# Optimization experiments

Measured on AMD Instinct MI355X. Metric: run time of the kernel, lower is better.

## Reference

```python
import jax, jax.numpy as jnp
import numpy as np

B, S, E, H = 4, 2048, 1024, 16
D = E // H  # head dim = 64


def setup_inputs() -> dict:
    key = jax.random.key(0)
    ks = jax.random.split(key, 9)
    sc = 1.0 / np.sqrt(E)
    x = jax.random.normal(ks[0], (B, S, E), dtype=jnp.float32)
    # causal mask: 1 = keep, 0 = masked -> -inf (matches masked_fill(mask==0, -inf))
    mask = jnp.broadcast_to(jnp.tril(jnp.ones((S, S), dtype=jnp.int32)), (B, S, S))
    return {
        "x": x,
        "mask": mask,
        "wq": jax.random.normal(ks[1], (E, E), dtype=jnp.float32) * sc,
        "bq": jax.random.normal(ks[2], (E,), dtype=jnp.float32) * sc,
        "wk": jax.random.normal(ks[3], (E, E), dtype=jnp.float32) * sc,
        "bk": jax.random.normal(ks[4], (E,), dtype=jnp.float32) * sc,
        "wv": jax.random.normal(ks[5], (E, E), dtype=jnp.float32) * sc,
        "bv": jax.random.normal(ks[6], (E,), dtype=jnp.float32) * sc,
        "wo": jax.random.normal(ks[7], (E, E), dtype=jnp.float32) * sc,
        "bo": jax.random.normal(ks[8], (E,), dtype=jnp.float32) * sc,
    }


def reference(x, mask, wq, bq, wk, bk, wv, bv, wo, bo):
    # nn.Linear: y = x @ W^T + b
    def proj(w, b):
        y = jnp.einsum('bse,fe->bsf', x, w) + b
        return y.reshape(B, S, H, D).transpose(0, 2, 1, 3)  # [B,H,S,D]

    q = proj(wq, bq)
    k = proj(wk, bk)
    v = proj(wv, bv)
    denom = jnp.asarray(np.sqrt(D), dtype=x.dtype)
    score = jnp.einsum('bhqd,bhkd->bhqk', q, k) / denom  # [B,H,S,S]
    score = jnp.where(mask[:, None, :, :] == 0, jnp.asarray(-jnp.inf, score.dtype), score)
    attn = jax.nn.softmax(score, axis=-1)
    out = jnp.einsum('bhqk,bhkd->bhqd', attn, v)  # [B,H,S,D]
    out = out.transpose(0, 2, 1, 3).reshape(B, S, E)
    return jnp.einsum('bse,fe->bsf', out, wo) + bo
```

## Files before the change

### kernel.cpp

```cpp
#include <hip/hip_runtime.h>
#include <cstdint>
#include <cstddef>

typedef unsigned short u16;
typedef __bf16 bf16;
typedef bf16 bf16x8 __attribute__((ext_vector_type(8)));
typedef bf16 bf16x4 __attribute__((ext_vector_type(4)));
typedef float f32x4 __attribute__((ext_vector_type(4)));
typedef u16 u16x8 __attribute__((ext_vector_type(8)));
typedef u16 u16x4 __attribute__((ext_vector_type(4)));

#define ASYNC16(g, l) __builtin_amdgcn_global_load_lds( \
    (const __attribute__((address_space(1))) void*)(g), \
    (__attribute__((address_space(3))) void*)(l), 16, 0, 0)

__device__ __forceinline__ u16 f2bf(float f) {
  bf16 h = (bf16)f;
  return __builtin_bit_cast(u16, h);
}

__device__ __forceinline__ u16x4 pk4(float a, float b, float c, float d) {
  bf16x4 v = { (bf16)a, (bf16)b, (bf16)c, (bf16)d };
  return __builtin_bit_cast(u16x4, v);
}

__device__ __forceinline__ void store_out(u16* p, float v) { *p = f2bf(v); }
__device__ __forceinline__ void store_out(float* p, float v) { *p = v; }

__device__ __forceinline__ f32x4 mfma16(bf16x8 a, bf16x8 b, f32x4 c) {
  return __builtin_amdgcn_mfma_f32_16x16x32_bf16(a, b, c, 0, 0, 0);
}

__global__ void prep(const float* __restrict__ x,  const float* __restrict__ wq,
                     const float* __restrict__ wk, const float* __restrict__ wv,
                     const float* __restrict__ wo, const float* __restrict__ bq,
                     const float* __restrict__ bk,
                     u16* __restrict__ xb, u16* __restrict__ wqkb,
                     u16* __restrict__ wvb, u16* __restrict__ wob,
                     float* __restrict__ bqk, float scl)
{
  const int bid = blockIdx.x, tid = threadIdx.x;
  if (bid < 8192) {
    int i = bid * 256 + tid;
    float4 v = ((const float4*)x)[i];
    ((u16x4*)xb)[i] = pk4(v.x, v.y, v.z, v.w);
  } else if (bid < 12288) {
    int wsel = (bid - 8192) >> 10;
    int i = ((bid - 8192) & 1023) * 256 + tid;
    const float* src = wsel == 0 ? wq : wsel == 1 ? wk : wsel == 2 ? wv : wo;
    u16* dst = wsel == 0 ? wqkb : wsel == 1 ? wqkb + 1048576 : wsel == 2 ? wvb : wob;
    float s = wsel == 0 ? scl : 1.0f;
    float4 v = ((const float4*)src)[i];
    ((u16x4*)dst)[i] = pk4(v.x * s, v.y * s, v.z * s, v.w * s);
  } else {
    for (int i = tid; i < 1024; i += 256) {
      bqk[i] = bq[i] * scl;
      bqk[1024 + i] = bk[i];
    }
  }
}

template <typename OutT>
__global__ __launch_bounds__(256, 2) void gemm_bt(
    const u16* __restrict__ A, const u16* __restrict__ Bm,
    const float* __restrict__ bias_col, const float* __restrict__ bias_row,
    OutT* __restrict__ C, int M, int N, int K)
{
  __shared__ u16 As[128 * 32];
  __shared__ u16 Bs[128 * 32];
  const int tid = threadIdx.x;
  const int w = tid >> 6, lane = tid & 63;
  const int q = lane >> 4, l15 = lane & 15;
  const int bm = blockIdx.x, bn = blockIdx.y;
  const int wr = w >> 1, wc = w & 1;

  const u16* gA = A + (size_t)(bm * 128 + w * 32 + (lane >> 2)) * K + (lane & 3) * 8;
  const u16* gB = Bm + (size_t)(bn * 128 + w * 32 + (lane >> 2)) * K + (lane & 3) * 8;
  u16* lA = As + w * 32 * 32;
  u16* lB = Bs + w * 32 * 32;

  f32x4 acc[4][4] = {};

  for (int k0 = 0; k0 < K; k0 += 32) {
    ASYNC16(gA + k0,          lA);
    ASYNC16(gA + k0 + 16 * K, lA + 16 * 32);
    ASYNC16(gB + k0,          lB);
    ASYNC16(gB + k0 + 16 * K, lB + 16 * 32);
    __syncthreads();
    bf16x8 af[4], bfr[4];
#pragma unroll
    for (int mt = 0; mt < 4; mt++)
      af[mt] = *(const bf16x8*)(As + (wr * 64 + mt * 16 + l15) * 32 + q * 8);
#pragma unroll
    for (int nt = 0; nt < 4; nt++)
      bfr[nt] = *(const bf16x8*)(Bs + (wc * 64 + nt * 16 + l15) * 32 + q * 8);
#pragma unroll
    for (int mt = 0; mt < 4; mt++)
#pragma unroll
      for (int nt = 0; nt < 4; nt++)
        acc[mt][nt] = mfma16(af[mt], bfr[nt], acc[mt][nt]);
    __syncthreads();
  }

#pragma unroll
  for (int nt = 0; nt < 4; nt++) {
    int c = bn * 128 + wc * 64 + nt * 16 + l15;
    float bc = bias_col ? bias_col[c] : 0.f;
#pragma unroll
    for (int mt = 0; mt < 4; mt++) {
      int r0 = bm * 128 + wr * 64 + mt * 16 + q * 4;
      f32x4 v = acc[mt][nt];
#pragma unroll
      for (int ri = 0; ri < 4; ri++) {
        float bv = bc + (bias_row ? bias_row[r0 + ri] : 0.f);
        store_out(&C[(size_t)(r0 + ri) * N + c], v[ri] + bv);
      }
    }
  }
}

__global__ __launch_bounds__(256, 2) void fattn(
    const u16* __restrict__ QK, const u16* __restrict__ VT, u16* __restrict__ ctx)
{
  __shared__ u16 Kt[128 * 64];
  __shared__ u16 Vt[64 * 128];

  const int tid = threadIdx.x;
  const int w = tid >> 6, lane = tid & 63;
  const int quad = lane >> 4, l15 = lane & 15;
  const int bx = blockIdx.x, h = blockIdx.y, b = blockIdx.z;
  const int base = (b & 2) << 2;
  const int tq = (b & 1) ? ((15 - bx + base) & 15) : ((bx + base) & 15);
  const int qbase = tq * 128 + w * 32;

  const int kr0 = tid >> 3, kcol = (tid & 7) ^ (kr0 & 7);
  const int vr0 = tid >> 4, vcol = (tid & 15) ^ (vr0 & 15);

  const u16* QKb = QK + (size_t)b * 2048 * 2048;
  const u16* Kg = QKb + 1024 + h * 64 + kcol * 8;
  const u16* Vg = VT + (size_t)(h * 64) * 8192 + b * 2048 + vcol * 8;

  u16* Pw = Kt + w * 2048;

  bf16x8 ones;
#pragma unroll
  for (int j = 0; j < 8; j++) ones[j] = (bf16)1.0f;

  bf16x8 qf[2][2];
#pragma unroll
  for (int mt = 0; mt < 2; mt++)
#pragma unroll
    for (int ks = 0; ks < 2; ks++)
      qf[mt][ks] = *(const bf16x8*)(QKb + (size_t)(qbase + mt * 16 + l15) * 2048 +
                                    h * 64 + ks * 32 + quad * 8);

  f32x4 oacc[4][2] = {};
  f32x4 lacc[2] = {};

  for (int t = 0; t <= tq; t++) {
    __syncthreads();
#pragma unroll
    for (int s = 0; s < 4; s++) {
      ASYNC16(Kg + (size_t)(t * 128 + s * 32 + kr0) * 2048, Kt + (s * 256 + w * 64) * 8);
      ASYNC16(Vg + (size_t)(s * 16 + vr0) * 8192 + t * 128, Vt + (s * 256 + w * 64) * 8);
    }
    __syncthreads();

    f32x4 st[2][8] = {};
#pragma unroll
    for (int ks = 0; ks < 2; ks++) {
      bf16x8 kf[8];
#pragma unroll
      for (int nt = 0; nt < 8; nt++) {
        int row = nt * 16 + l15;
        kf[nt] = *(const bf16x8*)(Kt + (row * 8 + ((ks * 4 + quad) ^ (row & 7))) * 8);
      }
#pragma unroll
      for (int nt = 0; nt < 8; nt++) {
        st[0][nt] = mfma16(kf[nt], qf[0][ks], st[0][nt]);
        st[1][nt] = mfma16(kf[nt], qf[1][ks], st[1][nt]);
      }
    }

    if (t == tq) {
#pragma unroll
      for (int mt = 0; mt < 2; mt++) {
        const int qg = qbase + mt * 16 + l15;
#pragma unroll
        for (int nt = 0; nt < 8; nt++)
#pragma unroll
          for (int r = 0; r < 4; r++)
            if (t * 128 + nt * 16 + quad * 4 + r > qg) st[mt][nt][r] = -3e38f;
      }
    }
#pragma unroll
    for (int mt = 0; mt < 2; mt++)
#pragma unroll
      for (int nt = 0; nt < 8; nt++)
#pragma unroll
        for (int r = 0; r < 4; r++)
          st[mt][nt][r] = exp2f(st[mt][nt][r]);

    __syncthreads();

#pragma unroll
    for (int hf = 0; hf < 2; hf++) {
#pragma unroll
      for (int mt = 0; mt < 2; mt++) {
        const int row = mt * 16 + l15;
#pragma unroll
        for (int n2 = 0; n2 < 4; n2++) {
          int nt = hf * 4 + n2;
          u16x4 pk = pk4(st[mt][nt][0], st[mt][nt][1], st[mt][nt][2], st[mt][nt][3]);
          int c = n2 * 2 + (quad >> 1);
          *(u16x4*)(Pw + (row << 6) + ((c ^ (row & 7)) << 3) + ((quad & 1) << 2)) = pk;
        }
      }
#pragma unroll
      for (int ks = 0; ks < 2; ks++) {
        const int c = ks * 4 + quad;
        bf16x8 pf0 = *(const bf16x8*)(Pw + (l15 << 6) + ((c ^ (l15 & 7)) << 3));
        bf16x8 pf1 = *(const bf16x8*)(Pw + ((16 + l15) << 6) + ((c ^ (l15 & 7)) << 3));
        lacc[0] = mfma16(ones, pf0, lacc[0]);
        lacc[1] = mfma16(ones, pf1, lacc[1]);
#pragma unroll
        for (int dt = 0; dt < 4; dt++) {
          int row = dt * 16 + l15;
          bf16x8 vf = *(const bf16x8*)(Vt + (row * 16 + ((hf * 8 + ks * 4 + quad) ^ (row & 15))) * 8);
          oacc[dt][0] = mfma16(vf, pf0, oacc[dt][0]);
          oacc[dt][1] = mfma16(vf, pf1, oacc[dt][1]);
        }
      }
    }
  }

#pragma unroll
  for (int mt = 0; mt < 2; mt++) {
    float rl = 1.0f / lacc[mt][0];
    size_t row = (size_t)b * 2048 + qbase + mt * 16 + l15;
#pragma unroll
    for (int dt = 0; dt < 4; dt++) {
      u16x4 o = pk4(oacc[dt][mt][0] * rl, oacc[dt][mt][1] * rl,
                    oacc[dt][mt][2] * rl, oacc[dt][mt][3] * rl);
      *(u16x4*)(ctx + row * 1024 + h * 64 + dt * 16 + quad * 4) = o;
    }
  }
}

extern "C" void kernel_launch(void* const* d_in, const int* in_sizes, int n_in,
                              void* d_out, int out_size, void* d_ws, size_t ws_size,
                              hipStream_t stream)
{
  const float* x  = (const float*)d_in[0];
  const float* wq = (const float*)d_in[2];
  const float* bq = (const float*)d_in[3];
  const float* wk = (const float*)d_in[4];
  const float* bk = (const float*)d_in[5];
  const float* wv = (const float*)d_in[6];
  const float* bv = (const float*)d_in[7];
  const float* wo = (const float*)d_in[8];
  const float* bo = (const float*)d_in[9];

  const float SCL = 0.125f * 1.44269504088896f;

  char* ws = (char*)d_ws;
  u16*   xb   = (u16*)(ws);
  u16*   ctx  = (u16*)(ws);
  u16*   wqkb = (u16*)(ws + 16777216);
  u16*   wvb  = (u16*)(ws + 20971520);
  u16*   wob  = (u16*)(ws + 23068672);
  float* bqk  = (float*)(ws + 25165824);
  u16*   qk   = (u16*)(ws + 25174016);
  u16*   vt   = (u16*)(ws + 58728448);
  float* out  = (float*)d_out;

  prep<<<12289, 256, 0, stream>>>(x, wq, wk, wv, wo, bq, bk,
                                  xb, wqkb, wvb, wob, bqk, SCL);

  gemm_bt<u16><<<dim3(64, 16), 256, 0, stream>>>(xb, wqkb, bqk, nullptr, qk, 8192, 2048, 1024);
  gemm_bt<u16><<<dim3(8, 64), 256, 0, stream>>>(wvb, xb, nullptr, bv, vt, 1024, 8192, 1024);
  fattn<<<dim3(16, 16, 4), 256, 0, stream>>>(qk, vt, ctx);
  gemm_bt<float><<<dim3(64, 8), 256, 0, stream>>>(ctx, wob, bo, nullptr, out, 8192, 1024, 1024);
}
```

Before: 338.1 us.

## Merge QK and V projection GEMMs into one launch; widen attention blocks to 8 waves

```diff
diff --git a/kernel.cpp b/kernel.cpp
--- a/kernel.cpp
+++ b/kernel.cpp
@@ -61,17 +61,15 @@
 }
 
 template <typename OutT>
-__global__ __launch_bounds__(256, 2) void gemm_bt(
+__device__ __forceinline__ void gemm_core(
+    u16* As, u16* Bs,
     const u16* __restrict__ A, const u16* __restrict__ Bm,
     const float* __restrict__ bias_col, const float* __restrict__ bias_row,
-    OutT* __restrict__ C, int M, int N, int K)
-{
-  __shared__ u16 As[128 * 32];
-  __shared__ u16 Bs[128 * 32];
+    OutT* __restrict__ C, int M, int N, int K, int bm, int bn)
+{
   const int tid = threadIdx.x;
   const int w = tid >> 6, lane = tid & 63;
   const int q = lane >> 4, l15 = lane & 15;
-  const int bm = blockIdx.x, bn = blockIdx.y;
   const int wr = w >> 1, wc = w & 1;
 
   const u16* gA = A + (size_t)(bm * 128 + w * 32 + (lane >> 2)) * K + (lane & 3) * 8;
@@ -119,28 +117,59 @@
   }
 }
 
-__global__ __launch_bounds__(256, 2) void fattn(
+template <typename OutT>
+__global__ __launch_bounds__(256, 2) void gemm_bt(
+    const u16* __restrict__ A, const u16* __restrict__ Bm,
+    const float* __restrict__ bias_col, const float* __restrict__ bias_row,
+    OutT* __restrict__ C, int M, int N, int K)
+{
+  __shared__ u16 As[128 * 32];
+  __shared__ u16 Bs[128 * 32];
+  gemm_core<OutT>(As, Bs, A, Bm, bias_col, bias_row, C, M, N, K,
+                  blockIdx.x, blockIdx.y);
+}
+
+__global__ __launch_bounds__(256, 2) void gemm_qkv(
+    const u16* __restrict__ xb, const u16* __restrict__ wqkb,
+    const u16* __restrict__ wvb, const float* __restrict__ bqk,
+    const float* __restrict__ bv, u16* __restrict__ qk, u16* __restrict__ vt)
+{
+  __shared__ u16 As[128 * 32];
+  __shared__ u16 Bs[128 * 32];
+  const int id = blockIdx.x;
+  if (id < 1024)
+    gemm_core<u16>(As, Bs, xb, wqkb, bqk, nullptr, qk, 8192, 2048, 1024,
+                   id & 63, id >> 6);
+  else {
+    const int j = id - 1024;
+    gemm_core<u16>(As, Bs, wvb, xb, nullptr, bv, vt, 1024, 8192, 1024,
+                   j & 7, j >> 3);
+  }
+}
+
+__global__ __launch_bounds__(512, 4) void fattn(
     const u16* __restrict__ QK, const u16* __restrict__ VT, u16* __restrict__ ctx)
 {
   __shared__ u16 Kt[128 * 64];
   __shared__ u16 Vt[64 * 128];
+  __shared__ u16 Pt[8 * 32 * 64];
 
   const int tid = threadIdx.x;
   const int w = tid >> 6, lane = tid & 63;
   const int quad = lane >> 4, l15 = lane & 15;
   const int bx = blockIdx.x, h = blockIdx.y, b = blockIdx.z;
-  const int base = (b & 2) << 2;
-  const int tq = (b & 1) ? ((15 - bx + base) & 15) : ((bx + base) & 15);
-  const int qbase = tq * 128 + w * 32;
-
-  const int kr0 = tid >> 3, kcol = (tid & 7) ^ (kr0 & 7);
-  const int vr0 = tid >> 4, vcol = (tid & 15) ^ (vr0 & 15);
+  const int P8[8] = {7, 0, 6, 1, 5, 2, 4, 3};
+  const int tq = (b & 2) ? 7 - P8[bx] : P8[bx];
+  const int qbase = tq * 256 + w * 32;
+
+  const int kr = tid >> 3, kc = (tid & 7) ^ (kr & 7);
+  const int vr = tid >> 4, vc = (tid & 15) ^ (vr & 15);
 
   const u16* QKb = QK + (size_t)b * 2048 * 2048;
-  const u16* Kg = QKb + 1024 + h * 64 + kcol * 8;
-  const u16* Vg = VT + (size_t)(h * 64) * 8192 + b * 2048 + vcol * 8;
-
-  u16* Pw = Kt + w * 2048;
+  const u16* Kg = QKb + 1024 + h * 64 + kc * 8;
+  const u16* Vg = VT + (size_t)(h * 64) * 8192 + b * 2048 + vc * 8;
+
+  u16* Pw = Pt + w * 2048;
 
   bf16x8 ones;
 #pragma unroll
@@ -157,12 +186,13 @@
   f32x4 oacc[4][2] = {};
   f32x4 lacc[2] = {};
 
-  for (int t = 0; t <= tq; t++) {
+  const int tmax = 2 * tq + 1;
+  for (int t = 0; t <= tmax; t++) {
     __syncthreads();
 #pragma unroll
-    for (int s = 0; s < 4; s++) {
-      ASYNC16(Kg + (size_t)(t * 128 + s * 32 + kr0) * 2048, Kt + (s * 256 + w * 64) * 8);
-      ASYNC16(Vg + (size_t)(s * 16 + vr0) * 8192 + t * 128, Vt + (s * 256 + w * 64) * 8);
+    for (int s = 0; s < 2; s++) {
+      ASYNC16(Kg + (size_t)(t * 128 + s * 64 + kr) * 2048, Kt + (s * 512 + w * 64) * 8);
+      ASYNC16(Vg + (size_t)(s * 32 + vr) * 8192 + t * 128,  Vt + (s * 512 + w * 64) * 8);
     }
     __syncthreads();
 
@@ -182,7 +212,7 @@
       }
     }
 
-    if (t == tq) {
+    if (t >= 2 * tq) {
 #pragma unroll
       for (int mt = 0; mt < 2; mt++) {
         const int qg = qbase + mt * 16 + l15;
@@ -200,8 +230,6 @@
 #pragma unroll
         for (int r = 0; r < 4; r++)
           st[mt][nt][r] = exp2f(st[mt][nt][r]);
-
-    __syncthreads();
 
 #pragma unroll
     for (int hf = 0; hf < 2; hf++) {
@@ -277,8 +305,7 @@
   prep<<<12289, 256, 0, stream>>>(x, wq, wk, wv, wo, bq, bk,
                                   xb, wqkb, wvb, wob, bqk, SCL);
 
-  gemm_bt<u16><<<dim3(64, 16), 256, 0, stream>>>(xb, wqkb, bqk, nullptr, qk, 8192, 2048, 1024);
-  gemm_bt<u16><<<dim3(8, 64), 256, 0, stream>>>(wvb, xb, nullptr, bv, vt, 1024, 8192, 1024);
-  fattn<<<dim3(16, 16, 4), 256, 0, stream>>>(qk, vt, ctx);
+  gemm_qkv<<<1536, 256, 0, stream>>>(xb, wqkb, wvb, bqk, bv, qk, vt);
+  fattn<<<dim3(8, 16, 4), 512, 0, stream>>>(qk, vt, ctx);
   gemm_bt<float><<<dim3(64, 8), 256, 0, stream>>>(ctx, wob, bo, nullptr, out, 8192, 1024, 1024);
 }
```

After: 438.7 us. +29.8%, slower.
